# Kernel optimization log

Hardware: AMD Instinct MI355X
Metric: run time of the kernel (lower is better)

## Reference

```python
import jax, jax.numpy as jnp
import numpy as np

W1 = 7          # half window
W2 = 2 * W1 + 1 # window size = 15
H = 4           # num heads
DH = 64         # head dim
DO = H * DH     # 256


def setup_inputs() -> dict:
    key = jax.random.key(0)
    ks = jax.random.split(key, 7)
    B, T, D = 2, 4096, 768
    s = 1.0 / np.sqrt(D).astype(np.float32)
    inputs = jax.random.normal(ks[0], (B, T, D), dtype=jnp.float32)
    Wq = jax.random.normal(ks[1], (DO, D), dtype=jnp.float32) * s
    bq = jax.random.normal(ks[2], (DO,), dtype=jnp.float32) * s
    Wv = jax.random.normal(ks[3], (DO, D), dtype=jnp.float32) * s
    bv = jax.random.normal(ks[4], (DO,), dtype=jnp.float32) * s
    pos_emb = jax.random.normal(ks[5], (W2, D), dtype=jnp.float32)
    return {"inputs": inputs, "Wq": Wq, "bq": bq, "Wv": Wv, "bv": bv, "pos_emb": pos_emb}


def reference(inputs, Wq, bq, Wv, bv, pos_emb):
    # Faithful to the torch module: k uses the *query* projection (source bug),
    # no softmax, no 1/sqrt(d) scaling.
    B, T, D = inputs.shape
    pad = jnp.pad(inputs, ((0, 0), (W1, W1), (0, 0)))  # [B, T+2*W1, D]
    # Project once on the padded sequence, then gather windows (linear ops
    # commute with the window gather; position bias added post-projection).
    q_pad = pad @ Wq.T + bq            # [B, T+2*W1, DO]
    v_pad = pad @ Wv.T + bv            # [B, T+2*W1, DO]
    pos_q = pos_emb @ Wq.T             # [W2, DO]  (query(window+pos) = query(window)+pos@Wq^T)
    pos_v = pos_emb @ Wv.T             # [W2, DO]
    idx = jnp.arange(T)[:, None] + jnp.arange(W2)[None, :]  # [T, W2]
    k = q_pad[:, idx] + pos_q          # [B, T, W2, DO]
    v = v_pad[:, idx] + pos_v          # [B, T, W2, DO]
    q = inputs @ Wq.T + bq             # [B, T, DO]
    qh = q.reshape(B, T, H, DH)
    kh = k.reshape(B, T, W2, H, DH)
    vh = v.reshape(B, T, W2, H, DH)
    scores = jnp.einsum('bthd,btwhd->bthw', qh, kh)   # [B, T, H, W2] (no softmax)
    ctx = jnp.einsum('bthw,btwhd->bthd', scores, vh)  # [B, T, H, DH]
    return ctx.reshape(B, T, DO)
```

## Files before the change

kernel.cpp:

```cpp
#include <hip/hip_runtime.h>

#define TPC   4110
#define MROWS 8220
#define MTOT  8235
#define MPAD  8320
#define KD    768

typedef __attribute__((ext_vector_type(8))) short short8;
typedef __attribute__((ext_vector_type(4))) float f32x4;

#define LOAD_LDS16(gp, lp)                                                   \
  __builtin_amdgcn_global_load_lds(                                          \
      (const __attribute__((address_space(1))) void*)(gp),                   \
      (__attribute__((address_space(3))) void*)(lp), 16, 0, 0)

__device__ inline unsigned bfr(float x) {
  unsigned u = __float_as_uint(x);
  return (u + 0x7FFFu + ((u >> 16) & 1u)) >> 16;
}
__device__ inline unsigned pack2(float a, float b) {
  return bfr(a) | (bfr(b) << 16);
}
__device__ inline float bflo(unsigned u) { return __uint_as_float(u << 16); }
__device__ inline float bfhi(unsigned u) { return __uint_as_float(u & 0xffff0000u); }

__global__ __launch_bounds__(256) void cast_ab(
    const float* __restrict__ inp, const float* __restrict__ Wq,
    const float* __restrict__ Wv, const float* __restrict__ pos,
    ushort* __restrict__ Abf, ushort* __restrict__ Wbf) {
  const int ACH = MPAD * 96;
  int gid = blockIdx.x * 256 + threadIdx.x;
  const float* src = nullptr;
  ushort* dst;
  if (gid < ACH) {
    int row = gid / 96, c = (gid - row * 96) * 8;
    dst = Abf + (size_t)row * KD + c;
    if (row < MROWS) {
      int b = row / TPC, t = row - b * TPC - 7;
      if (t >= 0 && t < 4096) src = inp + ((size_t)b * 4096 + t) * KD + c;
    } else if (row < MTOT) {
      src = pos + (size_t)(row - MROWS) * KD + c;
    }
  } else {
    int wid = gid - ACH;
    if (wid >= 512 * 96) return;
    int row = wid / 96, c = (wid - row * 96) * 8;
    dst = Wbf + (size_t)row * KD + c;
    src = (row < 256) ? Wq + (size_t)row * KD + c
                      : Wv + (size_t)(row - 256) * KD + c;
  }
  uint4 o;
  if (src) {
    float4 f0 = *(const float4*)src;
    float4 f1 = *(const float4*)(src + 4);
    o.x = pack2(f0.x, f0.y); o.y = pack2(f0.z, f0.w);
    o.z = pack2(f1.x, f1.y); o.w = pack2(f1.z, f1.w);
  } else {
    o.x = o.y = o.z = o.w = 0u;
  }
  *(uint4*)dst = o;
}

__global__ __launch_bounds__(256) void gemm_bf16(
    const ushort* __restrict__ Abf, const ushort* __restrict__ Wbf,
    const float* __restrict__ bq, const float* __restrict__ bv,
    ushort* __restrict__ q_out, ushort* __restrict__ v_out,
    ushort* __restrict__ pos_q, ushort* __restrict__ pos_v) {
  __shared__ ushort Al[64 * 64];
  __shared__ ushort Bl[128 * 64];
  const int tid = threadIdx.x;
  const int wave = tid >> 6, lane = tid & 63;
  const int ns = blockIdx.x;
  const int m0 = blockIdx.y * 64;
  const int wm = wave & 1, wn = wave >> 1;
  const int fr = lane & 15, quad = lane >> 4;

  const ushort* ag[2];
  #pragma unroll
  for (int i = 0; i < 2; i++) {
    int c = i * 256 + tid, row = c >> 3, kq = c & 7;
    ag[i] = Abf + (size_t)(m0 + row) * KD + ((kq ^ (row & 7)) * 8);
  }
  const ushort* bg[4];
  #pragma unroll
  for (int i = 0; i < 4; i++) {
    int c = i * 256 + tid, row = c >> 3, kq = c & 7;
    bg[i] = Wbf + (size_t)(ns * 128 + row) * KD + ((kq ^ (row & 7)) * 8);
  }
  ushort* al[2];
  ushort* bl[4];
  #pragma unroll
  for (int i = 0; i < 2; i++) al[i] = Al + (i * 256 + wave * 64) * 8;
  #pragma unroll
  for (int i = 0; i < 4; i++) bl[i] = Bl + (i * 256 + wave * 64) * 8;

  f32x4 acc[2][4];
  #pragma unroll
  for (int i = 0; i < 2; i++)
    #pragma unroll
    for (int j = 0; j < 4; j++) acc[i][j] = 0.0f;

  for (int k0 = 0; k0 < KD; k0 += 64) {
    #pragma unroll
    for (int i = 0; i < 2; i++) LOAD_LDS16(ag[i] + k0, al[i]);
    #pragma unroll
    for (int i = 0; i < 4; i++) LOAD_LDS16(bg[i] + k0, bl[i]);
    __syncthreads();
    short8 af[2][2], bf[2][4];
    #pragma unroll
    for (int ks = 0; ks < 2; ks++) {
      const int e = ((ks * 4 + quad) ^ (fr & 7)) * 8;
      #pragma unroll
      for (int i = 0; i < 2; i++)
        af[ks][i] = *(const short8*)(Al + (wm * 32 + i * 16 + fr) * 64 + e);
      #pragma unroll
      for (int j = 0; j < 4; j++)
        bf[ks][j] = *(const short8*)(Bl + (wn * 64 + j * 16 + fr) * 64 + e);
    }
    #pragma unroll
    for (int ks = 0; ks < 2; ks++)
      #pragma unroll
      for (int i = 0; i < 2; i++)
        #pragma unroll
        for (int j = 0; j < 4; j++)
          acc[i][j] = __builtin_amdgcn_mfma_f32_16x16x32_bf16(
              af[ks][i], bf[ks][j], acc[i][j], 0, 0, 0);
    __syncthreads();
  }

  const float* bias = (ns < 2) ? bq : bv;
  ushort* outp = (ns < 2) ? q_out : v_out;
  ushort* posp = (ns < 2) ? pos_q : pos_v;
  const int wbase = (ns & 1) * 128;
  #pragma unroll
  for (int j = 0; j < 4; j++) {
    const int colq = wbase + wn * 64 + j * 16 + fr;
    const int h = colq >> 6, d = colq & 63;
    const float bj = bias[colq];
    #pragma unroll
    for (int i = 0; i < 2; i++) {
      const int mb = m0 + wm * 32 + i * 16 + quad * 4;
      #pragma unroll
      for (int r = 0; r < 4; r++) {
        const int m = mb + r;
        if (m < MROWS) {
          int b = m / TPC, tp = m - b * TPC;
          outp[(((size_t)(b * 4 + h)) * TPC + tp) * 64 + d] =
              (ushort)bfr(acc[i][j][r] + bj);
        } else if (m < MTOT) {
          posp[(m - MROWS) * 256 + colq] = (ushort)bfr(acc[i][j][r]);
        }
      }
    }
  }
}

__global__ __launch_bounds__(256) void win_attn4(
    const ushort* __restrict__ q_out, const ushort* __restrict__ v_out,
    const ushort* __restrict__ pos_q, const ushort* __restrict__ pos_v,
    float* __restrict__ out) {
  __shared__ __align__(16) float ks[78][68];
  __shared__ __align__(16) float vs[78][68];
  __shared__ __align__(16) float pq[15][68];
  __shared__ __align__(16) float pv[15][68];
  const int tid = threadIdx.x;
  const int bh = blockIdx.x >> 6, tile = blockIdx.x & 63;
  const int b = bh >> 2, h = bh & 3;
  const int t0 = tile * 64;

  const size_t slab = (((size_t)(b * 4 + h)) * TPC + t0) * 64;
  for (int idx = tid; idx < 624; idx += 256) {
    int row = idx >> 3, c8 = (idx & 7) * 8;
    uint4 kc = *(const uint4*)(q_out + slab + idx * 8);
    ks[row][c8 + 0] = bflo(kc.x); ks[row][c8 + 1] = bfhi(kc.x);
    ks[row][c8 + 2] = bflo(kc.y); ks[row][c8 + 3] = bfhi(kc.y);
    ks[row][c8 + 4] = bflo(kc.z); ks[row][c8 + 5] = bfhi(kc.z);
    ks[row][c8 + 6] = bflo(kc.w); ks[row][c8 + 7] = bfhi(kc.w);
    uint4 vc = *(const uint4*)(v_out + slab + idx * 8);
    vs[row][c8 + 0] = bflo(vc.x); vs[row][c8 + 1] = bfhi(vc.x);
    vs[row][c8 + 2] = bflo(vc.y); vs[row][c8 + 3] = bfhi(vc.y);
    vs[row][c8 + 4] = bflo(vc.z); vs[row][c8 + 5] = bfhi(vc.z);
    vs[row][c8 + 6] = bflo(vc.w); vs[row][c8 + 7] = bfhi(vc.w);
  }
  if (tid < 120) {
    int row = tid >> 3, c8 = (tid & 7) * 8;
    uint4 qc = *(const uint4*)(pos_q + row * 256 + h * 64 + c8);
    pq[row][c8 + 0] = bflo(qc.x); pq[row][c8 + 1] = bfhi(qc.x);
    pq[row][c8 + 2] = bflo(qc.y); pq[row][c8 + 3] = bfhi(qc.y);
    pq[row][c8 + 4] = bflo(qc.z); pq[row][c8 + 5] = bfhi(qc.z);
    pq[row][c8 + 6] = bflo(qc.w); pq[row][c8 + 7] = bfhi(qc.w);
    uint4 vc = *(const uint4*)(pos_v + row * 256 + h * 64 + c8);
    pv[row][c8 + 0] = bflo(vc.x); pv[row][c8 + 1] = bfhi(vc.x);
    pv[row][c8 + 2] = bflo(vc.y); pv[row][c8 + 3] = bfhi(vc.y);
    pv[row][c8 + 4] = bflo(vc.z); pv[row][c8 + 5] = bfhi(vc.z);
    pv[row][c8 + 6] = bflo(vc.w); pv[row][c8 + 7] = bfhi(vc.w);
  }
  __syncthreads();

  const int tl = tid >> 2, qtr = tid & 3, d0 = qtr * 16;
  float4 qv[4];
  #pragma unroll
  for (int c = 0; c < 4; c++) qv[c] = *(float4*)&ks[tl + 7][d0 + c * 4];
  float4 ctx[4];
  #pragma unroll
  for (int c = 0; c < 4; c++) ctx[c] = make_float4(0.f, 0.f, 0.f, 0.f);

  #pragma unroll
  for (int w = 0; w < 15; w++) {
    float p = 0.f;
    #pragma unroll
    for (int c = 0; c < 4; c++) {
      float4 kk = *(float4*)&ks[tl + w][d0 + c * 4];
      float4 pp = *(float4*)&pq[w][d0 + c * 4];
      p += qv[c].x * (kk.x + pp.x) + qv[c].y * (kk.y + pp.y) +
           qv[c].z * (kk.z + pp.z) + qv[c].w * (kk.w + pp.w);
    }
    p += __shfl_xor(p, 1, 64);
    p += __shfl_xor(p, 2, 64);
    #pragma unroll
    for (int c = 0; c < 4; c++) {
      float4 vv = *(float4*)&vs[tl + w][d0 + c * 4];
      float4 pp = *(float4*)&pv[w][d0 + c * 4];
      ctx[c].x += p * (vv.x + pp.x);
      ctx[c].y += p * (vv.y + pp.y);
      ctx[c].z += p * (vv.z + pp.z);
      ctx[c].w += p * (vv.w + pp.w);
    }
  }
  size_t oo = ((size_t)(b * 4096 + t0 + tl)) * 256 + h * 64 + d0;
  #pragma unroll
  for (int c = 0; c < 4; c++) *(float4*)(out + oo + c * 4) = ctx[c];
}

extern "C" void kernel_launch(void* const* d_in, const int* in_sizes, int n_in,
                              void* d_out, int out_size, void* d_ws,
                              size_t ws_size, hipStream_t stream) {
  const float* inp = (const float*)d_in[0];
  const float* Wq  = (const float*)d_in[1];
  const float* bq  = (const float*)d_in[2];
  const float* Wv  = (const float*)d_in[3];
  const float* bv  = (const float*)d_in[4];
  const float* pos = (const float*)d_in[5];
  float* out = (float*)d_out;

  char* ws = (char*)d_ws;
  ushort* Abf   = (ushort*)ws;
  ushort* Wbf   = (ushort*)(ws + 12779520);
  ushort* q_out = (ushort*)(ws + 13565952);
  ushort* v_out = (ushort*)(ws + 17774592);
  ushort* pos_q = (ushort*)(ws + 21983232);
  ushort* pos_v = (ushort*)(ws + 21990912);

  const int cast_chunks = MPAD * 96 + 512 * 96;
  hipLaunchKernelGGL(cast_ab, dim3(cast_chunks / 256), dim3(256), 0, stream,
                     inp, Wq, Wv, pos, Abf, Wbf);
  hipLaunchKernelGGL(gemm_bf16, dim3(4, MPAD / 64), dim3(256), 0, stream,
                     Abf, Wbf, bq, bv, q_out, v_out, pos_q, pos_v);
  hipLaunchKernelGGL(win_attn4, dim3(2 * 4 * 64), dim3(256), 0, stream,
                     q_out, v_out, pos_q, pos_v, out);
}
```

Before: 110.7 us.

## Double-buffer GEMM LDS tiles and remap workgroups across XCDs

The bf16 projection GEMM now keeps two LDS buffers, so the global-to-LDS load for the next K tile is issued before the MFMAs run on the current tile. This halves the barriers per K step and hides load latency behind compute. The 2D grid becomes a 1D grid of 520 blocks with an index remap, intended to give each XCD a contiguous range of M tiles so neighbouring blocks share the A and W tiles in L2. LDS use doubles per block, which may lower occupancy.

```diff
diff --git a/kernel.cpp b/kernel.cpp
--- a/kernel.cpp
+++ b/kernel.cpp
@@ -66,12 +66,14 @@
     const float* __restrict__ bq, const float* __restrict__ bv,
     ushort* __restrict__ q_out, ushort* __restrict__ v_out,
     ushort* __restrict__ pos_q, ushort* __restrict__ pos_v) {
-  __shared__ ushort Al[64 * 64];
-  __shared__ ushort Bl[128 * 64];
+  __shared__ ushort Al[2][64 * 64];
+  __shared__ ushort Bl[2][128 * 64];
   const int tid = threadIdx.x;
   const int wave = tid >> 6, lane = tid & 63;
-  const int ns = blockIdx.x;
-  const int m0 = blockIdx.y * 64;
+  const int lin = blockIdx.x;
+  const int wg = (lin & 7) * 65 + (lin >> 3);
+  const int ns = wg & 3;
+  const int m0 = (wg >> 2) * 64;
   const int wm = wave & 1, wn = wave >> 1;
   const int fr = lane & 15, quad = lane >> 4;
 
@@ -87,12 +89,6 @@
     int c = i * 256 + tid, row = c >> 3, kq = c & 7;
     bg[i] = Wbf + (size_t)(ns * 128 + row) * KD + ((kq ^ (row & 7)) * 8);
   }
-  ushort* al[2];
-  ushort* bl[4];
-  #pragma unroll
-  for (int i = 0; i < 2; i++) al[i] = Al + (i * 256 + wave * 64) * 8;
-  #pragma unroll
-  for (int i = 0; i < 4; i++) bl[i] = Bl + (i * 256 + wave * 64) * 8;
 
   f32x4 acc[2][4];
   #pragma unroll
@@ -100,33 +96,59 @@
     #pragma unroll
     for (int j = 0; j < 4; j++) acc[i][j] = 0.0f;
 
-  for (int k0 = 0; k0 < KD; k0 += 64) {
-    #pragma unroll
-    for (int i = 0; i < 2; i++) LOAD_LDS16(ag[i] + k0, al[i]);
-    #pragma unroll
-    for (int i = 0; i < 4; i++) LOAD_LDS16(bg[i] + k0, bl[i]);
+#define STAGE(b, k0)                                                         \
+  do {                                                                       \
+    _Pragma("unroll")                                                        \
+    for (int i = 0; i < 2; i++)                                              \
+      LOAD_LDS16(ag[i] + (k0), &Al[b][0] + (i * 256 + wave * 64) * 8);       \
+    _Pragma("unroll")                                                        \
+    for (int i = 0; i < 4; i++)                                              \
+      LOAD_LDS16(bg[i] + (k0), &Bl[b][0] + (i * 256 + wave * 64) * 8);       \
+  } while (0)
+
+#define COMPUTE(b)                                                           \
+  do {                                                                       \
+    short8 afr[2][2], bfrag[2][4];                                           \
+    _Pragma("unroll")                                                        \
+    for (int ks = 0; ks < 2; ks++) {                                         \
+      const int e = ((ks * 4 + quad) ^ (fr & 7)) * 8;        \
+      _Pragma("unroll")                                                      \
+      for (int i = 0; i < 2; i++)                                            \
+        afr[ks][i] =                                                         \
+            *(const short8*)(&Al[b][0] + (wm * 32 + i * 16 + fr) * 64 + e);  \
+      _Pragma("unroll")                                                      \
+      for (int j = 0; j < 4; j++)                                            \
+        bfrag[ks][j] =                                                       \
+            *(const short8*)(&Bl[b][0] + (wn * 64 + j * 16 + fr) * 64 + e);  \
+    }                                                                        \
+    _Pragma("unroll")                                                        \
+    for (int ks = 0; ks < 2; ks++)                                           \
+      _Pragma("unroll")                                                      \
+      for (int i = 0; i < 2; i++)                                            \
+        _Pragma("unroll")                                                    \
+        for (int j = 0; j < 4; j++)                                          \
+          acc[i][j] = __builtin_amdgcn_mfma_f32_16x16x32_bf16(               \
+              afr[ks][i], bfrag[ks][j], acc[i][j], 0, 0, 0);                 \
+  } while (0)
+
+  STAGE(0, 0);
+  __syncthreads();
+  #pragma unroll 1
+  for (int k0 = 0; k0 < 640; k0 += 128) {
+    STAGE(1, k0 + 64);
+    COMPUTE(0);
     __syncthreads();
-    short8 af[2][2], bf[2][4];
-    #pragma unroll
-    for (int ks = 0; ks < 2; ks++) {
-      const int e = ((ks * 4 + quad) ^ (fr & 7)) * 8;
-      #pragma unroll
-      for (int i = 0; i < 2; i++)
-        af[ks][i] = *(const short8*)(Al + (wm * 32 + i * 16 + fr) * 64 + e);
-      #pragma unroll
-      for (int j = 0; j < 4; j++)
-        bf[ks][j] = *(const short8*)(Bl + (wn * 64 + j * 16 + fr) * 64 + e);
-    }
-    #pragma unroll
-    for (int ks = 0; ks < 2; ks++)
-      #pragma unroll
-      for (int i = 0; i < 2; i++)
-        #pragma unroll
-        for (int j = 0; j < 4; j++)
-          acc[i][j] = __builtin_amdgcn_mfma_f32_16x16x32_bf16(
-              af[ks][i], bf[ks][j], acc[i][j], 0, 0, 0);
+    STAGE(0, k0 + 128);
+    COMPUTE(1);
     __syncthreads();
   }
+  STAGE(1, 704);
+  COMPUTE(0);
+  __syncthreads();
+  COMPUTE(1);
+
+#undef STAGE
+#undef COMPUTE
 
   const float* bias = (ns < 2) ? bq : bv;
   ushort* outp = (ns < 2) ? q_out : v_out;
@@ -254,7 +276,7 @@
   const int cast_chunks = MPAD * 96 + 512 * 96;
   hipLaunchKernelGGL(cast_ab, dim3(cast_chunks / 256), dim3(256), 0, stream,
                      inp, Wq, Wv, pos, Abf, Wbf);
-  hipLaunchKernelGGL(gemm_bf16, dim3(4, MPAD / 64), dim3(256), 0, stream,
+  hipLaunchKernelGGL(gemm_bf16, dim3(520), dim3(256), 0, stream,
                      Abf, Wbf, bq, bv, q_out, v_out, pos_q, pos_v);
   hipLaunchKernelGGL(win_attn4, dim3(2 * 4 * 64), dim3(256), 0, stream,
                      q_out, v_out, pos_q, pos_v, out);
```

After: 109.7 us. No clear change (-0.9%).
